# Performance work log

Hardware: AMD Instinct MI355X
Metric: run time of the kernel (lower is better)

Reference implementation:

```python
import jax, jax.numpy as jnp
import numpy as np

B, T, D = 256, 256, 128
H, L = 384, 12
C = H // L  # chunk_size
G = 4 * H + 2 * L  # gate projection width


def setup_inputs() -> dict:
    key = jax.random.key(0)
    k1, k2, k3, k4 = jax.random.split(key, 4)
    x = jax.random.normal(k1, (B, T, D), dtype=jnp.float32)
    time = jax.random.uniform(k2, (B, T), dtype=jnp.float32)
    # torch Linear: y = z @ W.T + b; store transposed weights directly.
    Wk = jax.random.normal(k3, (D + 1, G), dtype=jnp.float32) * (1.0 / np.sqrt(D + 1))
    bk = jnp.zeros((G,), dtype=jnp.float32)
    Wr = jax.random.normal(k4, (H + 1, G), dtype=jnp.float32) * (1.0 / np.sqrt(H + 1))
    br = jnp.zeros((G,), dtype=jnp.float32)
    return {"x": x, "time": time, "Wk": Wk, "bk": bk, "Wr": Wr, "br": br}


def _cumax_l2r(z):
    return jnp.cumsum(jax.nn.softmax(z, axis=-1), axis=-1)


def _cumax_r2l(z):
    zf = jnp.flip(z, axis=-1)
    return jnp.flip(jnp.cumsum(jax.nn.softmax(zf, axis=-1), axis=-1), axis=-1)


def reference(x, time, Wk, bk, Wr, br):
    def step(carry, xt_tt):
        c_last, h_last = carry  # each [B, H]
        xt, tt = xt_tt          # [B, D], [B]
        tt = tt[:, None]        # [B, 1]
        x_out = (jnp.concatenate([xt, tt], axis=-1) @ Wk + bk
                 + jnp.concatenate([h_last, tt], axis=-1) @ Wr + br)  # [B, G]
        f_master = _cumax_l2r(x_out[:, :L])[:, :, None]       # [B, L, 1]
        i_master = _cumax_r2l(x_out[:, L:2 * L])[:, :, None]  # [B, L, 1]
        g = x_out[:, 2 * L:].reshape(-1, 4 * L, C)
        f_gate = jax.nn.sigmoid(g[:, :L])
        i_gate = jax.nn.sigmoid(g[:, L:2 * L])
        o_gate = jax.nn.sigmoid(g[:, 2 * L:3 * L])
        c_in = jnp.tanh(g[:, 3 * L:])
        cl = c_last.reshape(-1, L, C)
        overlap = f_master * i_master
        c_out = (overlap * (f_gate * cl + i_gate * c_in)
                 + (f_master - overlap) * cl
                 + (i_master - overlap) * c_in)
        h_out = (o_gate * jnp.tanh(c_out)).reshape(-1, H)
        c_out = c_out.reshape(-1, H)
        return (c_out, h_out), h_out

    init = (jnp.zeros((x.shape[0], H), x.dtype), jnp.zeros((x.shape[0], H), x.dtype))
    xs = (jnp.swapaxes(x, 0, 1), jnp.swapaxes(time, 0, 1))  # time-major
    _, hs = jax.lax.scan(step, init, xs)  # [T, B, H]
    return jnp.swapaxes(hs, 0, 1)  # [B, T, H]
```

## Files before the change

kernel.cpp:

```cpp
#include <hip/hip_runtime.h>
#include <hip/hip_cooperative_groups.h>

namespace cg = cooperative_groups;

typedef __bf16 bf16;
typedef __bf16 bf16x8 __attribute__((ext_vector_type(8)));
typedef float f32x4 __attribute__((ext_vector_type(4)));

#define Bsz 256
#define Tsz 256
#define Dsz 128
#define Hsz 384
#define Lsz 12
#define Gsz 1560
#define Ksz 512
#define STR 520
#define NCOL 128
#define CST 132
#define MT 16
#define JT 24
#define FSTRIDE 32

#define OFF_B   0
#define OFF_A   (NCOL*STR*2)
#define OFF_FM  (OFF_A + MT*STR*2)
#define OFF_IM  (OFF_FM + MT*Lsz*4)
#define OFF_TB  (OFF_IM + MT*Lsz*4)
#define OFF_WL  (OFF_TB + MT*4)
#define OFF_BI  (OFF_WL + NCOL*4)
#define OFF_CS  (OFF_BI + NCOL*4)
#define SMEM_BYTES (OFF_CS + MT*JT*4)

__device__ unsigned g_flags[256 * FSTRIDE];

__device__ __forceinline__ int map_gcol(int col, int jb) {
    if (col < 24) return col;
    int r = col - 24;
    int blk = r / 24;
    int jj = r - blk * 24;
    return 24 + blk * Hsz + jb + jj;
}

__device__ __forceinline__ float sigm(float v) { return 1.0f / (1.0f + expf(-v)); }

__device__ __forceinline__ float ldf(const void* p, size_t i, bool f32) {
    return f32 ? ((const float*)p)[i] : (float)((const bf16*)p)[i];
}

__global__ __launch_bounds__(256, 1) void stagenet_kernel(
    const void* __restrict__ x, const void* __restrict__ tim,
    const void* __restrict__ Wk, const void* __restrict__ bk,
    const void* __restrict__ Wr, const void* __restrict__ br,
    void* __restrict__ out)
{
    extern __shared__ char smem[];
    bf16*  Bl = (bf16*)(smem + OFF_B);
    float* Cl = (float*)(smem + OFF_B);
    bf16*  Al = (bf16*)(smem + OFF_A);
    float* FM = (float*)(smem + OFF_FM);
    float* IM = (float*)(smem + OFF_IM);
    float* TB = (float*)(smem + OFF_TB);
    float* WL = (float*)(smem + OFF_WL);
    float* BI = (float*)(smem + OFF_BI);
    float* CS = (float*)(smem + OFF_CS);

    const int tid = threadIdx.x;
    const int wg  = blockIdx.x;
    const int mg  = wg >> 4;
    const int ng  = wg & 15;
    const int b0  = mg * MT;
    const int jb  = ng * JT;
    const int grp = mg * 16;

    int insane = 0;
    {
        const unsigned short* wb = (const unsigned short*)Wk;
        for (int i = 0; i < 64; ++i) {
            unsigned short u = wb[i];
            int e = (u >> 7) & 0xFF;
            if ((e < 90 || e > 140) && u != 0) insane++;
        }
    }
    const bool isF32 = insane > 8;

    for (int u = tid; u < NCOL * Ksz; u += 256) {
        int col = u & (NCOL - 1);
        int k   = u >> 7;
        bf16 v = (bf16)0.0f;
        if (col < 120) {
            int gcol = map_gcol(col, jb);
            float f = (k < Dsz) ? ldf(Wk, (size_t)k * Gsz + gcol, isF32)
                                : ldf(Wr, (size_t)(k - Dsz) * Gsz + gcol, isF32);
            v = (bf16)f;
        }
        Bl[col * STR + k] = v;
    }
    for (int col = tid; col < NCOL; col += 256) {
        float wl = 0.f, bi = 0.f;
        if (col < 120) {
            int gcol = map_gcol(col, jb);
            wl = ldf(Wk, (size_t)Dsz * Gsz + gcol, isF32) + ldf(Wr, (size_t)Hsz * Gsz + gcol, isF32);
            bi = ldf(bk, gcol, isF32) + ldf(br, gcol, isF32);
        }
        WL[col] = wl; BI[col] = bi;
    }
    for (int i = tid; i < MT * JT; i += 256) CS[i] = 0.f;

    if (tid == 0)
        __hip_atomic_store(&g_flags[wg * FSTRIDE], 0u,
                           __ATOMIC_RELAXED, __HIP_MEMORY_SCOPE_AGENT);

    __syncthreads();
    cg::grid_group grid = cg::this_grid();
    grid.sync();
    __builtin_amdgcn_fence(__ATOMIC_ACQUIRE, "agent");

    const int lane = tid & 63;
    const int wv   = tid >> 6;
    const int m16  = lane & 15;
    const int quad = lane >> 4;
    const int n0   = (2 * wv) * 16 + m16;
    const int n1   = (2 * wv + 1) * 16 + m16;

    bf16x8 Bf0[16], Bf1[16];
    #pragma unroll
    for (int ks = 0; ks < 16; ++ks) {
        Bf0[ks] = *(const bf16x8*)(Bl + n0 * STR + ks * 32 + quad * 8);
        Bf1[ks] = *(const bf16x8*)(Bl + n1 * STR + ks * 32 + quad * 8);
    }
    __syncthreads();

    for (int t = 0; t < Tsz; ++t) {
        {
            int m = tid >> 4, q = tid & 15;
            bf16x8 val;
            size_t base = ((size_t)(b0 + m) * Tsz + t) * Dsz + q * 8;
            if (isF32) {
                const float* s = (const float*)x + base;
                #pragma unroll
                for (int j = 0; j < 8; ++j) val[j] = (bf16)s[j];
            } else {
                val = *(const bf16x8*)((const bf16*)x + base);
            }
            *(bf16x8*)(Al + m * STR + q * 8) = val;
        }
        if (t == 0) {
            for (int u = tid; u < MT * 48; u += 256) {
                int m = u / 48, q = u - m * 48;
                bf16x8 z;
                #pragma unroll
                for (int j = 0; j < 8; ++j) z[j] = (bf16)0.0f;
                *(bf16x8*)(Al + m * STR + 128 + q * 8) = z;
            }
        }
        if (tid < MT) TB[tid] = ldf(tim, (size_t)(b0 + tid) * Tsz + t, isF32);

        if (t > 0) {
            if (wv == 0) {
                const unsigned target = (unsigned)t;
                unsigned v = target;
                for (;;) {
                    if (lane < 16)
                        v = __hip_atomic_load(&g_flags[(grp + lane) * FSTRIDE],
                                              __ATOMIC_RELAXED, __HIP_MEMORY_SCOPE_AGENT);
                    if (!__any(v < target)) break;
                    __builtin_amdgcn_s_sleep(1);
                }
            }
            __syncthreads();

            for (int u = tid; u < MT * 48; u += 256) {
                int m = u / 48, q = u - m * 48;
                bf16x8 val;
                size_t base = ((size_t)(b0 + m) * Tsz + (t - 1)) * Hsz + q * 8;
                if (isF32) {
                    const float* s = (const float*)out + base;
                    #pragma unroll
                    for (int j = 0; j < 8; ++j) val[j] = (bf16)s[j];
                } else {
                    val = *(const bf16x8*)((const bf16*)out + base);
                }
                *(bf16x8*)(Al + m * STR + 128 + q * 8) = val;
            }
        }
        __syncthreads();

        f32x4 a0 = {0.f, 0.f, 0.f, 0.f}, a1 = {0.f, 0.f, 0.f, 0.f};
        #pragma unroll
        for (int ks = 0; ks < 16; ++ks) {
            bf16x8 av = *(const bf16x8*)(Al + m16 * STR + ks * 32 + quad * 8);
            a0 = __builtin_amdgcn_mfma_f32_16x16x32_bf16(av, Bf0[ks], a0, 0, 0, 0);
            a1 = __builtin_amdgcn_mfma_f32_16x16x32_bf16(av, Bf1[ks], a1, 0, 0, 0);
        }

        #pragma unroll
        for (int r = 0; r < 4; ++r) {
            Cl[(quad * 4 + r) * CST + (2 * wv) * 16 + m16]     = a0[r];
            Cl[(quad * 4 + r) * CST + (2 * wv + 1) * 16 + m16] = a1[r];
        }
        __syncthreads();

        if (tid < MT) {
            const int m = tid;
            const float tb = TB[m];
            float z[24];
            #pragma unroll
            for (int i = 0; i < 24; ++i)
                z[i] = Cl[m * CST + i] + BI[i] + tb * WL[i];
            float mx = z[0];
            #pragma unroll
            for (int i = 1; i < 12; ++i) mx = fmaxf(mx, z[i]);
            float e[12], s = 0.f;
            #pragma unroll
            for (int i = 0; i < 12; ++i) { e[i] = expf(z[i] - mx); s += e[i]; }
            float inv = 1.f / s, run = 0.f;
            #pragma unroll
            for (int i = 0; i < 12; ++i) { run += e[i]; FM[m * Lsz + i] = run * inv; }
            mx = z[12];
            #pragma unroll
            for (int i = 13; i < 24; ++i) mx = fmaxf(mx, z[i]);
            s = 0.f;
            #pragma unroll
            for (int i = 0; i < 12; ++i) { e[i] = expf(z[12 + i] - mx); s += e[i]; }
            inv = 1.f / s; run = 0.f;
            #pragma unroll
            for (int i = 11; i >= 0; --i) { run += e[i]; IM[m * Lsz + i] = run * inv; }
        }
        __syncthreads();

        for (int fi = tid; fi < MT * JT; fi += 256) {
            int m = fi / JT;
            int j = fi - m * JT;
            int gj = jb + j;
            int l = gj >> 5;
            float tb = TB[m];
            float vf = Cl[m * CST + 24 + j] + BI[24 + j] + tb * WL[24 + j];
            float vi = Cl[m * CST + 48 + j] + BI[48 + j] + tb * WL[48 + j];
            float vo = Cl[m * CST + 72 + j] + BI[72 + j] + tb * WL[72 + j];
            float vc = Cl[m * CST + 96 + j] + BI[96 + j] + tb * WL[96 + j];
            float fg = sigm(vf);
            float ig = sigm(vi);
            float og = sigm(vo);
            float ci = tanhf(vc);
            float fm = FM[m * Lsz + l];
            float im = IM[m * Lsz + l];
            float ov = fm * im;
            float co = CS[fi];
            float cn = ov * (fg * co + ig * ci) + (fm - ov) * co + (im - ov) * ci;
            CS[fi] = cn;
            float hv = og * tanhf(cn);
            size_t oidx = ((size_t)(b0 + m) * Tsz + t) * Hsz + gj;
            if (isF32) {
                __hip_atomic_store((float*)out + oidx, hv,
                                   __ATOMIC_RELAXED, __HIP_MEMORY_SCOPE_AGENT);
            } else {
                bf16 hb = (bf16)hv;
                __hip_atomic_store((unsigned short*)out + oidx,
                                   __builtin_bit_cast(unsigned short, hb),
                                   __ATOMIC_RELAXED, __HIP_MEMORY_SCOPE_AGENT);
            }
        }

        if (t < Tsz - 1) {
            __builtin_amdgcn_s_waitcnt(0);
            __syncthreads();
            if (tid == 0)
                __hip_atomic_store(&g_flags[wg * FSTRIDE], (unsigned)(t + 1),
                                   __ATOMIC_RELAXED, __HIP_MEMORY_SCOPE_AGENT);
        }
    }
}

extern "C" void kernel_launch(void* const* d_in, const int* in_sizes, int n_in,
                              void* d_out, int out_size, void* d_ws, size_t ws_size,
                              hipStream_t stream) {
    const void* x  = d_in[0];
    const void* tm = d_in[1];
    const void* Wk = d_in[2];
    const void* bk = d_in[3];
    const void* Wr = d_in[4];
    const void* br = d_in[5];

    hipFuncSetAttribute(reinterpret_cast<const void*>(&stagenet_kernel),
                        hipFuncAttributeMaxDynamicSharedMemorySize, SMEM_BYTES);

    void* args[] = {(void*)&x, (void*)&tm, (void*)&Wk, (void*)&bk,
                    (void*)&Wr, (void*)&br, (void*)&d_out};
    hipLaunchCooperativeKernel(stagenet_kernel, dim3(256), dim3(256),
                               args, SMEM_BYTES, stream);
}
```

Baseline: 1.765 ms.

## Exchange hidden state through tagged 64-bit workspace slots instead of flag polling

Adds a workspace exchange buffer where each block publishes its bf16 hidden-state slice packed three values per 64-bit word, tagged with the timestep in the top 16 bits. Consumers poll those tagged words directly and write them into shared memory, so the separate flag barrier and the re-read of the output tensor disappear. Transcendental functions also switch to fast __expf-based sigmoid and tanh. Correctness of the exchange relies on the workspace being large enough and not holding a stale matching tag at start (there is no initial grid sync or clear), and the four-slot ring assumes producers never run more than a few steps ahead.

```diff
diff --git a/kernel.cpp b/kernel.cpp
--- a/kernel.cpp
+++ b/kernel.cpp
@@ -6,6 +6,7 @@
 typedef __bf16 bf16;
 typedef __bf16 bf16x8 __attribute__((ext_vector_type(8)));
 typedef float f32x4 __attribute__((ext_vector_type(4)));
+typedef unsigned long long u64;
 
 #define Bsz 256
 #define Tsz 256
@@ -20,6 +21,9 @@
 #define MT 16
 #define JT 24
 #define FSTRIDE 32
+#define NBLK 128
+#define SLOTS 4
+#define EXCH_BYTES ((size_t)SLOTS * Bsz * NBLK * 8)
 
 #define OFF_B   0
 #define OFF_A   (NCOL*STR*2)
@@ -29,7 +33,8 @@
 #define OFF_WL  (OFF_TB + MT*4)
 #define OFF_BI  (OFF_WL + NCOL*4)
 #define OFF_CS  (OFF_BI + NCOL*4)
-#define SMEM_BYTES (OFF_CS + MT*JT*4)
+#define OFF_HS  (OFF_CS + MT*JT*4)
+#define SMEM_BYTES (OFF_HS + MT*26*2)
 
 __device__ unsigned g_flags[256 * FSTRIDE];
 
@@ -41,7 +46,12 @@
     return 24 + blk * Hsz + jb + jj;
 }
 
-__device__ __forceinline__ float sigm(float v) { return 1.0f / (1.0f + expf(-v)); }
+__device__ __forceinline__ float sigm(float v) { return 1.0f / (1.0f + __expf(-v)); }
+__device__ __forceinline__ float ftanh(float v) {
+    float xc = fminf(fmaxf(v, -10.f), 10.f);
+    float e = __expf(2.f * xc);
+    return (e - 1.f) / (e + 1.f);
+}
 
 __device__ __forceinline__ float ldf(const void* p, size_t i, bool f32) {
     return f32 ? ((const float*)p)[i] : (float)((const bf16*)p)[i];
@@ -51,7 +61,7 @@
     const void* __restrict__ x, const void* __restrict__ tim,
     const void* __restrict__ Wk, const void* __restrict__ bk,
     const void* __restrict__ Wr, const void* __restrict__ br,
-    void* __restrict__ out)
+    void* __restrict__ out, u64* __restrict__ exch)
 {
     extern __shared__ char smem[];
     bf16*  Bl = (bf16*)(smem + OFF_B);
@@ -63,6 +73,7 @@
     float* WL = (float*)(smem + OFF_WL);
     float* BI = (float*)(smem + OFF_BI);
     float* CS = (float*)(smem + OFF_CS);
+    unsigned short* HS = (unsigned short*)(smem + OFF_HS);
 
     const int tid = threadIdx.x;
     const int wg  = blockIdx.x;
@@ -71,6 +82,7 @@
     const int b0  = mg * MT;
     const int jb  = ng * JT;
     const int grp = mg * 16;
+    const bool useEx = (exch != nullptr);
 
     int insane = 0;
     {
@@ -106,14 +118,17 @@
     }
     for (int i = tid; i < MT * JT; i += 256) CS[i] = 0.f;
 
-    if (tid == 0)
-        __hip_atomic_store(&g_flags[wg * FSTRIDE], 0u,
-                           __ATOMIC_RELAXED, __HIP_MEMORY_SCOPE_AGENT);
-
-    __syncthreads();
-    cg::grid_group grid = cg::this_grid();
-    grid.sync();
-    __builtin_amdgcn_fence(__ATOMIC_ACQUIRE, "agent");
+    if (!useEx) {
+        if (tid == 0)
+            __hip_atomic_store(&g_flags[wg * FSTRIDE], 0u,
+                               __ATOMIC_RELAXED, __HIP_MEMORY_SCOPE_AGENT);
+        __syncthreads();
+        cg::grid_group grid = cg::this_grid();
+        grid.sync();
+        __builtin_amdgcn_fence(__ATOMIC_ACQUIRE, "agent");
+    } else {
+        __syncthreads();
+    }
 
     const int lane = tid & 63;
     const int wv   = tid >> 6;
@@ -156,31 +171,66 @@
         if (tid < MT) TB[tid] = ldf(tim, (size_t)(b0 + tid) * Tsz + t, isF32);
 
         if (t > 0) {
-            if (wv == 0) {
-                const unsigned target = (unsigned)t;
-                unsigned v = target;
-                for (;;) {
-                    if (lane < 16)
-                        v = __hip_atomic_load(&g_flags[(grp + lane) * FSTRIDE],
-                                              __ATOMIC_RELAXED, __HIP_MEMORY_SCOPE_AGENT);
-                    if (!__any(v < target)) break;
-                    __builtin_amdgcn_s_sleep(1);
-                }
-            }
-            __syncthreads();
-
-            for (int u = tid; u < MT * 48; u += 256) {
-                int m = u / 48, q = u - m * 48;
-                bf16x8 val;
-                size_t base = ((size_t)(b0 + m) * Tsz + (t - 1)) * Hsz + q * 8;
-                if (isF32) {
-                    const float* s = (const float*)out + base;
+            if (useEx) {
+                const int slot = (t - 1) & (SLOTS - 1);
+                const unsigned want = (unsigned)(t - 1);
+                const u64* pp[8];
+                u64 v[8];
+                #pragma unroll
+                for (int i = 0; i < 8; ++i) {
+                    int g = tid + 256 * i;
+                    int m = g >> 7, blk = g & 127;
+                    pp[i] = &exch[((size_t)slot * Bsz + (b0 + m)) * NBLK + blk];
+                    v[i] = __hip_atomic_load(pp[i], __ATOMIC_RELAXED,
+                                             __HIP_MEMORY_SCOPE_AGENT);
+                }
+                unsigned pend = 0xFFu;
+                while (pend) {
                     #pragma unroll
-                    for (int j = 0; j < 8; ++j) val[j] = (bf16)s[j];
-                } else {
-                    val = *(const bf16x8*)((const bf16*)out + base);
-                }
-                *(bf16x8*)(Al + m * STR + 128 + q * 8) = val;
+                    for (int i = 0; i < 8; ++i) {
+                        if ((pend >> i) & 1) {
+                            if ((unsigned)(v[i] >> 48) == want) {
+                                int g = tid + 256 * i;
+                                int m = g >> 7, blk = g & 127;
+                                unsigned short* d =
+                                    (unsigned short*)(Al + m * STR + 128 + blk * 3);
+                                d[0] = (unsigned short)v[i];
+                                d[1] = (unsigned short)(v[i] >> 16);
+                                d[2] = (unsigned short)(v[i] >> 32);
+                                pend &= ~(1u << i);
+                            } else {
+                                v[i] = __hip_atomic_load(pp[i], __ATOMIC_RELAXED,
+                                                         __HIP_MEMORY_SCOPE_AGENT);
+                            }
+                        }
+                    }
+                }
+            } else {
+                if (wv == 0) {
+                    const unsigned target = (unsigned)t;
+                    unsigned v = target;
+                    for (;;) {
+                        if (lane < 16)
+                            v = __hip_atomic_load(&g_flags[(grp + lane) * FSTRIDE],
+                                                  __ATOMIC_RELAXED, __HIP_MEMORY_SCOPE_AGENT);
+                        if (!__any(v < target)) break;
+                        __builtin_amdgcn_s_sleep(1);
+                    }
+                }
+                __syncthreads();
+                for (int u = tid; u < MT * 48; u += 256) {
+                    int m = u / 48, q = u - m * 48;
+                    bf16x8 val;
+                    size_t base = ((size_t)(b0 + m) * Tsz + (t - 1)) * Hsz + q * 8;
+                    if (isF32) {
+                        const float* s = (const float*)out + base;
+                        #pragma unroll
+                        for (int j = 0; j < 8; ++j) val[j] = (bf16)s[j];
+                    } else {
+                        val = *(const bf16x8*)((const bf16*)out + base);
+                    }
+                    *(bf16x8*)(Al + m * STR + 128 + q * 8) = val;
+                }
             }
         }
         __syncthreads();
@@ -192,7 +242,6 @@
             a0 = __builtin_amdgcn_mfma_f32_16x16x32_bf16(av, Bf0[ks], a0, 0, 0, 0);
             a1 = __builtin_amdgcn_mfma_f32_16x16x32_bf16(av, Bf1[ks], a1, 0, 0, 0);
         }
-
         #pragma unroll
         for (int r = 0; r < 4; ++r) {
             Cl[(quad * 4 + r) * CST + (2 * wv) * 16 + m16]     = a0[r];
@@ -212,7 +261,7 @@
             for (int i = 1; i < 12; ++i) mx = fmaxf(mx, z[i]);
             float e[12], s = 0.f;
             #pragma unroll
-            for (int i = 0; i < 12; ++i) { e[i] = expf(z[i] - mx); s += e[i]; }
+            for (int i = 0; i < 12; ++i) { e[i] = __expf(z[i] - mx); s += e[i]; }
             float inv = 1.f / s, run = 0.f;
             #pragma unroll
             for (int i = 0; i < 12; ++i) { run += e[i]; FM[m * Lsz + i] = run * inv; }
@@ -221,7 +270,7 @@
             for (int i = 13; i < 24; ++i) mx = fmaxf(mx, z[i]);
             s = 0.f;
             #pragma unroll
-            for (int i = 0; i < 12; ++i) { e[i] = expf(z[12 + i] - mx); s += e[i]; }
+            for (int i = 0; i < 12; ++i) { e[i] = __expf(z[12 + i] - mx); s += e[i]; }
             inv = 1.f / s; run = 0.f;
             #pragma unroll
             for (int i = 11; i >= 0; --i) { run += e[i]; IM[m * Lsz + i] = run * inv; }
@@ -241,32 +290,54 @@
             float fg = sigm(vf);
             float ig = sigm(vi);
             float og = sigm(vo);
-            float ci = tanhf(vc);
+            float ci = ftanh(vc);
             float fm = FM[m * Lsz + l];
             float im = IM[m * Lsz + l];
             float ov = fm * im;
             float co = CS[fi];
             float cn = ov * (fg * co + ig * ci) + (fm - ov) * co + (im - ov) * ci;
             CS[fi] = cn;
-            float hv = og * tanhf(cn);
+            float hv = og * ftanh(cn);
+            bf16 hb = (bf16)hv;
             size_t oidx = ((size_t)(b0 + m) * Tsz + t) * Hsz + gj;
-            if (isF32) {
-                __hip_atomic_store((float*)out + oidx, hv,
-                                   __ATOMIC_RELAXED, __HIP_MEMORY_SCOPE_AGENT);
+            if (useEx) {
+                if (isF32) ((float*)out)[oidx] = hv;
+                else       ((bf16*)out)[oidx] = hb;
+                HS[m * 26 + j] = __builtin_bit_cast(unsigned short, hb);
             } else {
-                bf16 hb = (bf16)hv;
-                __hip_atomic_store((unsigned short*)out + oidx,
-                                   __builtin_bit_cast(unsigned short, hb),
-                                   __ATOMIC_RELAXED, __HIP_MEMORY_SCOPE_AGENT);
-            }
-        }
-
-        if (t < Tsz - 1) {
-            __builtin_amdgcn_s_waitcnt(0);
+                if (isF32) {
+                    __hip_atomic_store((float*)out + oidx, hv,
+                                       __ATOMIC_RELAXED, __HIP_MEMORY_SCOPE_AGENT);
+                } else {
+                    __hip_atomic_store((unsigned short*)out + oidx,
+                                       __builtin_bit_cast(unsigned short, hb),
+                                       __ATOMIC_RELAXED, __HIP_MEMORY_SCOPE_AGENT);
+                }
+            }
+        }
+
+        if (useEx) {
             __syncthreads();
-            if (tid == 0)
-                __hip_atomic_store(&g_flags[wg * FSTRIDE], (unsigned)(t + 1),
-                                   __ATOMIC_RELAXED, __HIP_MEMORY_SCOPE_AGENT);
+            if (t < Tsz - 1) {
+                for (int u2 = tid; u2 < MT * 8; u2 += 256) {
+                    int m = u2 >> 3, lb = u2 & 7;
+                    const unsigned short* hs = &HS[m * 26 + lb * 3];
+                    u64 vv = (u64)hs[0] | ((u64)hs[1] << 16) | ((u64)hs[2] << 32)
+                           | ((u64)(unsigned)t << 48);
+                    int blk = ng * 8 + lb;
+                    __hip_atomic_store(
+                        &exch[((size_t)(t & (SLOTS - 1)) * Bsz + (b0 + m)) * NBLK + blk],
+                        vv, __ATOMIC_RELAXED, __HIP_MEMORY_SCOPE_AGENT);
+                }
+            }
+        } else {
+            if (t < Tsz - 1) {
+                __builtin_amdgcn_s_waitcnt(0);
+                __syncthreads();
+                if (tid == 0)
+                    __hip_atomic_store(&g_flags[wg * FSTRIDE], (unsigned)(t + 1),
+                                       __ATOMIC_RELAXED, __HIP_MEMORY_SCOPE_AGENT);
+            }
         }
     }
 }
@@ -280,12 +351,13 @@
     const void* bk = d_in[3];
     const void* Wr = d_in[4];
     const void* br = d_in[5];
+    u64* exch = (ws_size >= EXCH_BYTES) ? (u64*)d_ws : nullptr;
 
     hipFuncSetAttribute(reinterpret_cast<const void*>(&stagenet_kernel),
                         hipFuncAttributeMaxDynamicSharedMemorySize, SMEM_BYTES);
 
     void* args[] = {(void*)&x, (void*)&tm, (void*)&Wk, (void*)&bk,
-                    (void*)&Wr, (void*)&br, (void*)&d_out};
+                    (void*)&Wr, (void*)&br, (void*)&d_out, (void*)&exch};
     hipLaunchCooperativeKernel(stagenet_kernel, dim3(256), dim3(256),
                                args, SMEM_BYTES, stream);
 }
```

Result: faster. 1.712 ms (-3.0%).
